# Performance work log

Hardware: AMD Instinct MI355X
Metric: run time of the kernel (lower is better)

## Reference

```python
import jax, jax.numpy as jnp
import numpy as np

N_NODES = 50000
N_EDGES = 1600000
D = 128


def setup_inputs() -> dict:
    key = jax.random.key(0)
    k1, k2, k3, k4 = jax.random.split(key, 4)
    x = jax.random.normal(k1, (N_NODES, D), dtype=jnp.float32)
    edge_index = jax.random.randint(k2, (2, N_EDGES), 0, N_NODES, dtype=jnp.int64)
    # Xavier-uniform-like W; B is zeros in torch init but use small random for grad coverage
    limit = float(np.sqrt(6.0 / (D + D)))
    W = jax.random.uniform(k3, (D, D), dtype=jnp.float32, minval=-limit, maxval=limit)
    B = jax.random.uniform(k4, (D, D), dtype=jnp.float32, minval=-limit, maxval=limit)
    return {"x": x, "edge_index": edge_index, "W": W, "B": B}


def reference(x, edge_index, W, B):
    sources = edge_index[0]
    destinations = edge_index[1]
    # gather messages from source nodes, scatter-add into destinations
    messages = x[sources]  # [E, D]
    aggregated = jax.ops.segment_sum(messages, destinations, num_segments=N_NODES)  # [N, D]
    deg = jax.ops.segment_sum(jnp.ones((N_EDGES,), dtype=x.dtype), destinations, num_segments=N_NODES)
    deg = jnp.where(deg == 0, jnp.asarray(1.0, dtype=x.dtype), deg)
    mean_msg = aggregated / deg[:, None]
    # update: messages @ W.T + x @ B.T
    return mean_msg @ W.T + x @ B.T
```

## Files before the change

### kernel.cpp

```cpp
#include <hip/hip_runtime.h>
#include <hip/hip_bf16.h>

#define NN 50000
#define NE 1600000
#define DD 128
#define NPB 64
#define NBK 782
#define MAXB 2560
#define CHUNK 6144
#define NCB 261
#define WS 136

typedef __attribute__((ext_vector_type(8))) short short8;
typedef __attribute__((ext_vector_type(4))) float f32x4;

__device__ inline unsigned short to_bf16(float v) {
    __hip_bfloat16 h = __float2bfloat16(v);
    return __builtin_bit_cast(unsigned short, h);
}

__global__ __launch_bounds__(1024) void convscatter_k(const int* __restrict__ ei,
                                                      const float* __restrict__ x,
                                                      unsigned int* __restrict__ xb,
                                                      int* __restrict__ gcursor,
                                                      int* __restrict__ ebuf) {
    __shared__ int stg[CHUNK];
    __shared__ int h[NBK];
    __shared__ int lbase[NBK];
    __shared__ int gb[NBK];
    __shared__ int hcur[NBK];
    __shared__ int sc[1024];
    const int t = threadIdx.x;
    const int e0 = blockIdx.x * CHUNK;
    const int ec = min(CHUNK, NE - e0);

    for (int i = t; i < NBK; i += 1024) h[i] = 0;
    __syncthreads();

    unsigned int w2[6];
    #pragma unroll
    for (int u = 0; u < 6; ++u) {
        int i = u * 1024 + t;
        if (i < ec) {
            int src = ei[e0 + i];
            int dst = ei[NE + e0 + i];
            int b = dst >> 6;
            w2[u] = ((unsigned)b << 22) | ((unsigned)src << 6) | (unsigned)(dst & 63);
            atomicAdd(&h[b], 1);
        } else w2[u] = 0xFFFFFFFFu;
    }

    {
        int gid = blockIdx.x * 1024 + t;
        const int total4 = NN * DD / 4;
        for (int i = gid; i < total4; i += NCB * 1024) {
            float4 v = ((const float4*)x)[i];
            int p = __builtin_amdgcn_cvt_pk_fp8_f32(v.x, v.y, 0, false);
            p = __builtin_amdgcn_cvt_pk_fp8_f32(v.z, v.w, p, true);
            xb[i] = (unsigned)p;
        }
    }
    __syncthreads();

    int v = (t < NBK) ? h[t] : 0;
    sc[t] = v;
    __syncthreads();
    #pragma unroll
    for (int o = 1; o < 1024; o <<= 1) {
        int a = (t >= o) ? sc[t - o] : 0;
        __syncthreads();
        sc[t] += a;
        __syncthreads();
    }
    int excl = sc[t] - v;
    if (t < NBK) {
        lbase[t] = excl;
        hcur[t] = excl;
        gb[t] = v ? t * MAXB + atomicAdd(&gcursor[t], v) : 0;
    }
    __syncthreads();

    #pragma unroll
    for (int u = 0; u < 6; ++u) {
        if (w2[u] != 0xFFFFFFFFu) {
            int b = w2[u] >> 22;
            int pos = atomicAdd(&hcur[b], 1);
            stg[pos] = (int)w2[u];
        }
    }
    __syncthreads();

    for (int i = t; i < ec; i += 1024) {
        unsigned int w = (unsigned)stg[i];
        int b = w >> 22;
        ebuf[gb[b] + (i - lbase[b])] = (int)(w & 0x3FFFFFu);
    }
}

__global__ __launch_bounds__(512) void sortagg_k(const unsigned int* __restrict__ xb,
                                                 const int* __restrict__ ebuf,
                                                 const int* __restrict__ gcursor,
                                                 unsigned int* __restrict__ meanb) {
    __shared__ int stg[MAXB];
    __shared__ unsigned short srt[MAXB];
    __shared__ int cnt[NPB], cur[NPB], off[NPB + 1];
    const int b = blockIdx.x, t = threadIdx.x;
    const int n = gcursor[b];
    const int* __restrict__ slab = ebuf + (size_t)b * MAXB;
    for (int i = t; i < n; i += 512) stg[i] = slab[i];
    if (t < NPB) cnt[t] = 0;
    __syncthreads();
    for (int i = t; i < n; i += 512) atomicAdd(&cnt[stg[i] & 63], 1);
    __syncthreads();
    if (t < 64) {
        int v = cnt[t];
        int s = v;
        #pragma unroll
        for (int o = 1; o < 64; o <<= 1) {
            int u = __shfl_up(s, o);
            if (t >= o) s += u;
        }
        cur[t] = s - v;
        off[t] = s - v;
        if (t == 63) off[64] = s;
    }
    __syncthreads();
    for (int i = t; i < n; i += 512) {
        int w = stg[i];
        int pos = atomicAdd(&cur[w & 63], 1);
        srt[pos] = (unsigned short)(w >> 6);
    }
    __syncthreads();

    const int wv = t >> 6, lane = t & 63;
    const int half = lane >> 5, il = lane & 31;
    #pragma unroll
    for (int q = 0; q < 8; ++q) {
        int ln = wv + q * 8;
        int s0 = off[ln], s1 = off[ln + 1];
        float a0 = 0.f, a1 = 0.f, a2 = 0.f, a3 = 0.f;
        int i = s0;
        for (; i + 16 <= s1; i += 16) {
            unsigned int u[8];
            #pragma unroll
            for (int k = 0; k < 8; ++k)
                u[k] = xb[(size_t)srt[i + 2 * k + half] * 32 + il];
            #pragma unroll
            for (int k = 0; k < 8; ++k) {
                auto lo = __builtin_amdgcn_cvt_pk_f32_fp8((int)u[k], false);
                auto hi = __builtin_amdgcn_cvt_pk_f32_fp8((int)u[k], true);
                a0 += lo[0]; a1 += lo[1]; a2 += hi[0]; a3 += hi[1];
            }
        }
        for (; i < s1; i += 2) {
            int e = i + half;
            unsigned int u = (e < s1) ? xb[(size_t)srt[e] * 32 + il] : 0u;
            auto lo = __builtin_amdgcn_cvt_pk_f32_fp8((int)u, false);
            auto hi = __builtin_amdgcn_cvt_pk_f32_fp8((int)u, true);
            a0 += lo[0]; a1 += lo[1]; a2 += hi[0]; a3 += hi[1];
        }
        a0 += __shfl_xor(a0, 32);
        a1 += __shfl_xor(a1, 32);
        a2 += __shfl_xor(a2, 32);
        a3 += __shfl_xor(a3, 32);
        int node = b * NPB + ln;
        if (half == 0 && node < NN) {
            float inv = 1.0f / fmaxf((float)(s1 - s0), 1.0f);
            unsigned lo = (unsigned)to_bf16(a0 * inv) | ((unsigned)to_bf16(a1 * inv) << 16);
            unsigned hi = (unsigned)to_bf16(a2 * inv) | ((unsigned)to_bf16(a3 * inv) << 16);
            ((uint2*)meanb)[(size_t)node * 32 + il] = make_uint2(lo, hi);
        }
    }
}

__global__ __launch_bounds__(256) void gemm_mfma_k(const unsigned short* __restrict__ meanb,
                                                   const float* __restrict__ x,
                                                   const float* __restrict__ W,
                                                   const float* __restrict__ Bm,
                                                   float* __restrict__ out) {
    __shared__ unsigned short Wt[DD * WS];
    __shared__ unsigned short Bt[DD * WS];
    const int tid = threadIdx.x;
    #pragma unroll
    for (int it = 0; it < 16; ++it) {
        int idx = it * 256 + tid;
        int n = idx >> 5;
        int k0 = (idx & 31) * 4;
        float4 w4 = ((const float4*)W)[idx];
        float4 b4 = ((const float4*)Bm)[idx];
        ushort4 wp, bp;
        wp.x = to_bf16(w4.x); wp.y = to_bf16(w4.y); wp.z = to_bf16(w4.z); wp.w = to_bf16(w4.w);
        bp.x = to_bf16(b4.x); bp.y = to_bf16(b4.y); bp.z = to_bf16(b4.z); bp.w = to_bf16(b4.w);
        *(ushort4*)&Wt[n * WS + k0] = wp;
        *(ushort4*)&Bt[n * WS + k0] = bp;
    }
    __syncthreads();

    const int wave = tid >> 6;
    const int lane = tid & 63;
    const int m = lane & 15;
    const int quad = lane >> 4;
    const int rowA = min(blockIdx.x * 64 + wave * 16 + m, NN - 1);

    f32x4 acc[8];
    #pragma unroll
    for (int nt = 0; nt < 8; ++nt) acc[nt] = (f32x4){0.f, 0.f, 0.f, 0.f};

    #pragma unroll
    for (int t = 0; t < 4; ++t) {
        const int k8 = t * 32 + quad * 8;
        short8 mf = *(const short8*)&meanb[(size_t)rowA * DD + k8];
        float xv[8];
        {
            const float4* xq = (const float4*)&x[(size_t)rowA * DD + k8];
            float4 b0 = xq[0], b1 = xq[1];
            xv[0] = b0.x; xv[1] = b0.y; xv[2] = b0.z; xv[3] = b0.w;
            xv[4] = b1.x; xv[5] = b1.y; xv[6] = b1.z; xv[7] = b1.w;
        }
        short8 xh, xl;
        #pragma unroll
        for (int j = 0; j < 8; ++j) {
            unsigned short g = to_bf16(xv[j]);
            xh[j] = (short)g;
            xl[j] = (short)to_bf16(xv[j] - __uint_as_float((unsigned)g << 16));
        }
        #pragma unroll
        for (int nt = 0; nt < 8; ++nt) {
            int nrow = nt * 16 + m;
            short8 wf = *(const short8*)&Wt[nrow * WS + k8];
            short8 bf = *(const short8*)&Bt[nrow * WS + k8];
            acc[nt] = __builtin_amdgcn_mfma_f32_16x16x32_bf16(xl, bf, acc[nt], 0, 0, 0);
            acc[nt] = __builtin_amdgcn_mfma_f32_16x16x32_bf16(mf, wf, acc[nt], 0, 0, 0);
            acc[nt] = __builtin_amdgcn_mfma_f32_16x16x32_bf16(xh, bf, acc[nt], 0, 0, 0);
        }
    }

    const int rowD0 = blockIdx.x * 64 + wave * 16 + quad * 4;
    #pragma unroll
    for (int nt = 0; nt < 8; ++nt) {
        #pragma unroll
        for (int r = 0; r < 4; ++r) {
            int row = rowD0 + r;
            if (row < NN) out[(size_t)row * DD + nt * 16 + m] = acc[nt][r];
        }
    }
}

extern "C" void kernel_launch(void* const* d_in, const int* in_sizes, int n_in,
                              void* d_out, int out_size, void* d_ws, size_t ws_size,
                              hipStream_t stream) {
    const float* x  = (const float*)d_in[0];
    const int*   ei = (const int*)d_in[1];
    const float* W  = (const float*)d_in[2];
    const float* Bm = (const float*)d_in[3];
    float* out = (float*)d_out;

    unsigned int* meanb = (unsigned int*)d_ws;
    unsigned int* xb    = meanb + (size_t)NN * 64;
    int* ebuf     = (int*)(xb + (size_t)NN * 32);
    int* gcursor  = ebuf + (size_t)NBK * MAXB;

    hipMemsetAsync(gcursor, 0, NBK * sizeof(int), stream);
    convscatter_k<<<NCB, 1024, 0, stream>>>(ei, x, xb, gcursor, ebuf);
    sortagg_k<<<NBK, 512, 0, stream>>>(xb, ebuf, gcursor, meanb);
    gemm_mfma_k<<<(NN + 63) / 64, 256, 0, stream>>>((const unsigned short*)meanb, x, W, Bm, out);
}
```

Measured before the change: 154.4 us.

## Use wave-shuffle scans, per-wave histograms, and deeper gather unrolling

The block-wide prefix scan in the scatter kernel, which used about 20 __syncthreads, is replaced by a two-level wave-shuffle scan that needs only two barriers. In the sort/aggregate kernel, the per-node count histogram is split into per-wave copies to reduce LDS atomic contention, and the copies are summed before the scan. The gather loop now issues 16 outstanding loads per iteration instead of 8, with an 8-load tail step, to raise memory-level parallelism at the cost of more registers.

```diff
diff --git a/kernel.cpp b/kernel.cpp
--- a/kernel.cpp
+++ b/kernel.cpp
@@ -29,8 +29,9 @@
     __shared__ int lbase[NBK];
     __shared__ int gb[NBK];
     __shared__ int hcur[NBK];
-    __shared__ int sc[1024];
+    __shared__ int wsum[16], wbase[16];
     const int t = threadIdx.x;
+    const int lane = t & 63, wv = t >> 6;
     const int e0 = blockIdx.x * CHUNK;
     const int ec = min(CHUNK, NE - e0);
 
@@ -63,17 +64,27 @@
     __syncthreads();
 
     int v = (t < NBK) ? h[t] : 0;
-    sc[t] = v;
-    __syncthreads();
-    #pragma unroll
-    for (int o = 1; o < 1024; o <<= 1) {
-        int a = (t >= o) ? sc[t - o] : 0;
-        __syncthreads();
-        sc[t] += a;
-        __syncthreads();
-    }
-    int excl = sc[t] - v;
+    int s = v;
+    #pragma unroll
+    for (int o = 1; o < 64; o <<= 1) {
+        int u = __shfl_up(s, o);
+        if (lane >= o) s += u;
+    }
+    if (lane == 63) wsum[wv] = s;
+    __syncthreads();
+    if (wv == 0 && lane < 16) {
+        int bv = wsum[lane];
+        int bs = bv;
+        #pragma unroll
+        for (int o = 1; o < 16; o <<= 1) {
+            int u = __shfl_up(bs, o);
+            if (lane >= o) bs += u;
+        }
+        wbase[lane] = bs - bv;
+    }
+    __syncthreads();
     if (t < NBK) {
+        int excl = s - v + wbase[wv];
         lbase[t] = excl;
         hcur[t] = excl;
         gb[t] = v ? t * MAXB + atomicAdd(&gcursor[t], v) : 0;
@@ -103,17 +114,21 @@
                                                  unsigned int* __restrict__ meanb) {
     __shared__ int stg[MAXB];
     __shared__ unsigned short srt[MAXB];
-    __shared__ int cnt[NPB], cur[NPB], off[NPB + 1];
+    __shared__ int cnt8[8][NPB];
+    __shared__ int cur[NPB], off[NPB + 1];
     const int b = blockIdx.x, t = threadIdx.x;
+    const int wv = t >> 6, lane = t & 63;
     const int n = gcursor[b];
     const int* __restrict__ slab = ebuf + (size_t)b * MAXB;
     for (int i = t; i < n; i += 512) stg[i] = slab[i];
-    if (t < NPB) cnt[t] = 0;
-    __syncthreads();
-    for (int i = t; i < n; i += 512) atomicAdd(&cnt[stg[i] & 63], 1);
+    if (lane < NPB) cnt8[wv][lane] = 0;
+    __syncthreads();
+    for (int i = t; i < n; i += 512) atomicAdd(&cnt8[wv][stg[i] & 63], 1);
     __syncthreads();
     if (t < 64) {
-        int v = cnt[t];
+        int v = 0;
+        #pragma unroll
+        for (int w = 0; w < 8; ++w) v += cnt8[w][t];
         int s = v;
         #pragma unroll
         for (int o = 1; o < 64; o <<= 1) {
@@ -132,7 +147,6 @@
     }
     __syncthreads();
 
-    const int wv = t >> 6, lane = t & 63;
     const int half = lane >> 5, il = lane & 31;
     #pragma unroll
     for (int q = 0; q < 8; ++q) {
@@ -140,7 +154,19 @@
         int s0 = off[ln], s1 = off[ln + 1];
         float a0 = 0.f, a1 = 0.f, a2 = 0.f, a3 = 0.f;
         int i = s0;
-        for (; i + 16 <= s1; i += 16) {
+        for (; i + 32 <= s1; i += 32) {
+            unsigned int u[16];
+            #pragma unroll
+            for (int k = 0; k < 16; ++k)
+                u[k] = xb[(size_t)srt[i + 2 * k + half] * 32 + il];
+            #pragma unroll
+            for (int k = 0; k < 16; ++k) {
+                auto lo = __builtin_amdgcn_cvt_pk_f32_fp8((int)u[k], false);
+                auto hi = __builtin_amdgcn_cvt_pk_f32_fp8((int)u[k], true);
+                a0 += lo[0]; a1 += lo[1]; a2 += hi[0]; a3 += hi[1];
+            }
+        }
+        if (i + 16 <= s1) {
             unsigned int u[8];
             #pragma unroll
             for (int k = 0; k < 8; ++k)
@@ -151,6 +177,7 @@
                 auto hi = __builtin_amdgcn_cvt_pk_f32_fp8((int)u[k], true);
                 a0 += lo[0]; a1 += lo[1]; a2 += hi[0]; a3 += hi[1];
             }
+            i += 16;
         }
         for (; i < s1; i += 2) {
             int e = i + half;
```

Result: no change. 154.0 us (-0.3%).
